# Optimization experiments

Measured on AMD Instinct MI355X. Metric: run time of the kernel, lower is better.

Reference implementation:

```python
import math
import jax
import jax.numpy as jnp
import numpy as np

N = 2_000_000
FOCAL = 1000.0
WIDTH = 1920.0
HEIGHT = 1080.0


def _quat_to_rot(q):
    # normalized quaternion (w, x, y, z) -> (N, 3, 3) rotation
    q = q / jnp.linalg.norm(q, axis=-1, keepdims=True)
    r, x, y, z = q[:, 0], q[:, 1], q[:, 2], q[:, 3]
    return jnp.stack([
        jnp.stack([1 - 2 * (y * y + z * z), 2 * (x * y - r * z), 2 * (x * z + r * y)], axis=-1),
        jnp.stack([2 * (x * y + r * z), 1 - 2 * (x * x + z * z), 2 * (y * z - r * x)], axis=-1),
        jnp.stack([2 * (x * z - r * y), 2 * (y * z + r * x), 1 - 2 * (x * x + y * y)], axis=-1),
    ], axis=1)


def _forward(points, quaternions, scales, colors, opacity, extrinsic, intrinsic,
             focal_x, focal_y, width, height, tile_size):
    fw, fh = float(width), float(height)
    # compute_fov_from_focal: fov = 2*atan(dim/(2*focal)); tan(fov/2)
    tan_fovX = math.tan(2.0 * math.atan(fw / (2.0 * focal_x)) / 2.0)
    tan_fovY = math.tan(2.0 * math.atan(fh / (2.0 * focal_y)) / 2.0)

    # 3D covariance: Sigma = (R S)(R S)^T
    R = _quat_to_rot(quaternions)
    M = R * scales[:, None, :]
    cov3d = M @ jnp.swapaxes(M, 1, 2)  # (N,3,3)

    ph = jnp.concatenate([points, jnp.ones_like(points[:, :1])], axis=1)  # (N,4)
    pc = ph @ extrinsic                         # camera space (N,4)
    zc = pc[:, 2]
    zmask = zc > 0.2
    z_safe = jnp.where(zmask, zc, 1.0)          # guard divisions for culled points
    x = jnp.clip(pc[:, 0] / z_safe, -1.3 * tan_fovX, 1.3 * tan_fovX) * zc
    y = jnp.clip(pc[:, 1] / z_safe, -1.3 * tan_fovY, 1.3 * tan_fovY) * zc

    zero = jnp.zeros_like(z_safe)
    j00 = focal_x / z_safe
    j02 = -(focal_x * x) / z_safe ** 2
    j11 = focal_y / z_safe
    j12 = -(focal_y * y) / z_safe ** 2
    J = jnp.stack([
        jnp.stack([j00, zero, j02], axis=-1),
        jnp.stack([zero, j11, j12], axis=-1),
        jnp.stack([zero, zero, zero], axis=-1)], axis=1)  # (N,3,3)

    Wm = extrinsic[:3, :3]
    T = jnp.einsum('ij,nkj->nik', Wm, J)        # W @ J^T, (N,3,3)
    C = jnp.swapaxes(T, 1, 2) @ jnp.swapaxes(cov3d, 1, 2) @ T
    a = C[:, 0, 0] + 0.3
    d = C[:, 1, 1] + 0.3
    b = C[:, 0, 1]
    c = C[:, 1, 0]
    cov2d = jnp.stack([jnp.stack([a, b], -1), jnp.stack([c, d], -1)], axis=1)  # (N,2,2)

    ndc = pc @ intrinsic
    w_safe = jnp.where(zmask, ndc[:, 3], 1.0)
    nx = ndc[:, 0] / w_safe
    ny = ndc[:, 1] / w_safe
    nz = ndc[:, 2]
    mask = (nz > 0.2) & (nx < 1.3) & (nx > -1.3) & (ny < 1.3) & (ny > -1.3)

    # analytic 2x2 inverse
    det = a * d - b * c
    det_safe = jnp.where(jnp.abs(det) < 1e-12, 1e-12, det)
    inv = jnp.stack([jnp.stack([d, -b], -1), jnp.stack([-c, a], -1)], axis=1) / det_safe[:, None, None]

    # radius from max eigenvalue of 2x2 covariance
    mid = 0.5 * (a + d)
    s = jnp.sqrt(jnp.maximum(mid * mid - det, 0.1))
    lmax = jnp.maximum(mid + s, mid - s)
    radius = jnp.ceil(3.0 * jnp.sqrt(jnp.maximum(lmax, 1e-6)))

    # ndc2Pix
    px = ((nx + 1.0) * fw - 1.0) * 0.5
    py = ((ny + 1.0) * fh - 1.0) * 0.5

    max_tx = math.ceil(fw / tile_size) - 1
    max_ty = math.ceil(fh / tile_size) - 1
    tlx = jnp.clip(((px - radius) / tile_size).astype(jnp.int32), 0, max_tx)
    tly = jnp.clip(((py - radius) / tile_size).astype(jnp.int32), 0, max_ty)
    brx = jnp.clip(((px + radius) / tile_size).astype(jnp.int32), 0, max_tx)
    bry = jnp.clip(((py + radius) / tile_size).astype(jnp.int32), 0, max_ty)
    span = jnp.maximum(brx + 1 - tlx, 1) * jnp.maximum(bry + 1 - tly, 1)
    tiles_touched = jnp.where(mask, span, 0)

    mean = jnp.stack([px, py, nz], axis=1)
    float_out = jnp.concatenate([
        mean,                      # 3: pixel-space mean + depth
        cov2d.reshape(-1, 4),      # 4
        inv.reshape(-1, 4),        # 4
        radius[:, None],           # 1
        colors,                    # 3
        opacity[:, None],          # 1
    ], axis=1)                     # (N,16)
    float_out = jnp.where(mask[:, None], float_out, 0.0)
    top_left = jnp.stack([tlx, tly])
    bottom_right = jnp.stack([brx, bry])
    return float_out, tiles_touched, top_left, bottom_right, mask


def setup_inputs() -> dict:
    key = jax.random.key(0)
    k = jax.random.split(key, 5)
    points = jax.random.normal(k[0], (N, 3), jnp.float32) * 2.0
    quaternions = jax.random.normal(k[1], (N, 4), jnp.float32)
    scales = jax.random.uniform(k[2], (N, 3), jnp.float32, 0.01, 0.1)
    colors = jax.random.uniform(k[3], (N, 3), jnp.float32)
    opacity = jax.random.normal(k[4], (N,), jnp.float32)
    # extrinsic is TRANSPOSED (translation in last row): camera 5 units back
    E = np.eye(4, dtype=np.float32)
    E[3, :3] = np.array([0.0, 0.0, 5.0], dtype=np.float32)
    # intrinsic (transposed OpenGL-style): w = z, z passed through
    tanX = WIDTH / (2.0 * FOCAL)
    tanY = HEIGHT / (2.0 * FOCAL)
    I = np.zeros((4, 4), dtype=np.float32)
    I[0, 0] = 1.0 / tanX
    I[1, 1] = 1.0 / tanY
    I[2, 2] = 1.0
    I[2, 3] = 1.0
    return {
        'points': points, 'quaternions': quaternions, 'scales': scales,
        'colors': colors, 'opacity': opacity,
        'extrinsic': jnp.asarray(E), 'intrinsic': jnp.asarray(I),
        'focal_x': 1000, 'focal_y': 1000, 'width': 1920, 'height': 1080,
        'tile_size': 16,
    }


def reference(points, quaternions, scales, colors, opacity, extrinsic, intrinsic,
              focal_x, focal_y, width, height, tile_size):
    return _forward(points, quaternions, scales, colors, opacity, extrinsic,
                    intrinsic, float(focal_x), float(focal_y), float(width),
                    float(height), int(tile_size))
```

## Files before the change

### kernel.cpp

```cpp
#include <hip/hip_runtime.h>
#include <math.h>

__global__ __launch_bounds__(256) void gs_fwd(
    const float* __restrict__ points,
    const float* __restrict__ quats,
    const float* __restrict__ scales,
    const float* __restrict__ colors,
    const float* __restrict__ opac,
    const float* __restrict__ E,
    const float* __restrict__ I,
    const int* __restrict__ p_fx,
    const int* __restrict__ p_fy,
    const int* __restrict__ p_w,
    const int* __restrict__ p_h,
    const int* __restrict__ p_tile,
    float* __restrict__ out,
    int N)
{
    const int i = blockIdx.x * blockDim.x + threadIdx.x;
    if (i >= N) return;

    const float fx = (float)p_fx[0];
    const float fy = (float)p_fy[0];
    const float fw = (float)p_w[0];
    const float fh = (float)p_h[0];
    const float ftile = (float)p_tile[0];
    const float rtile = __builtin_amdgcn_rcpf(ftile);

    const float tanX = fw / (2.0f * fx);
    const float tanY = fh / (2.0f * fy);
    const int max_tx = (int)ceilf(fw * rtile) - 1;
    const int max_ty = (int)ceilf(fh * rtile) - 1;

    const float4 q = reinterpret_cast<const float4*>(quats)[i];
    const float rq = rsqrtf(q.x*q.x + q.y*q.y + q.z*q.z + q.w*q.w);
    const float qr = q.x * rq;
    const float qx = q.y * rq;
    const float qy = q.z * rq;
    const float qz = q.w * rq;

    const float r00 = 1.0f - 2.0f * (qy*qy + qz*qz);
    const float r01 = 2.0f * (qx*qy - qr*qz);
    const float r02 = 2.0f * (qx*qz + qr*qy);
    const float r10 = 2.0f * (qx*qy + qr*qz);
    const float r11 = 1.0f - 2.0f * (qx*qx + qz*qz);
    const float r12 = 2.0f * (qy*qz - qr*qx);
    const float r20 = 2.0f * (qx*qz - qr*qy);
    const float r21 = 2.0f * (qy*qz + qr*qx);
    const float r22 = 1.0f - 2.0f * (qx*qx + qy*qy);

    const float s0 = scales[3*i + 0];
    const float s1 = scales[3*i + 1];
    const float s2 = scales[3*i + 2];

    const float m00 = r00*s0, m01 = r01*s1, m02 = r02*s2;
    const float m10 = r10*s0, m11 = r11*s1, m12 = r12*s2;
    const float m20 = r20*s0, m21 = r21*s1, m22 = r22*s2;

    const float S00 = m00*m00 + m01*m01 + m02*m02;
    const float S01 = m00*m10 + m01*m11 + m02*m12;
    const float S02 = m00*m20 + m01*m21 + m02*m22;
    const float S11 = m10*m10 + m11*m11 + m12*m12;
    const float S12 = m10*m20 + m11*m21 + m12*m22;
    const float S22 = m20*m20 + m21*m21 + m22*m22;

    const float p0 = points[3*i + 0];
    const float p1 = points[3*i + 1];
    const float p2 = points[3*i + 2];
    const float pc0 = p0*E[0]  + p1*E[4]  + p2*E[8]  + E[12];
    const float pc1 = p0*E[1]  + p1*E[5]  + p2*E[9]  + E[13];
    const float pc2 = p0*E[2]  + p1*E[6]  + p2*E[10] + E[14];
    const float pc3 = p0*E[3]  + p1*E[7]  + p2*E[11] + E[15];

    const float zc = pc2;
    const bool  zmask = zc > 0.2f;
    const float z_safe = zmask ? zc : 1.0f;
    const float rz = __builtin_amdgcn_rcpf(z_safe);

    const float limX = 1.3f * tanX;
    const float limY = 1.3f * tanY;
    const float xx = fminf(fmaxf(pc0 * rz, -limX), limX) * zc;
    const float yy = fminf(fmaxf(pc1 * rz, -limY), limY) * zc;

    const float j00 = fx * rz;
    const float j02 = -(fx * xx) * rz * rz;
    const float j11 = fy * rz;
    const float j12 = -(fy * yy) * rz * rz;

    const float t00 = E[0]*j00 + E[2]*j02;
    const float t01 = E[4]*j00 + E[6]*j02;
    const float t02 = E[8]*j00 + E[10]*j02;
    const float t10 = E[1]*j11 + E[2]*j12;
    const float t11 = E[5]*j11 + E[6]*j12;
    const float t12 = E[9]*j11 + E[10]*j12;

    const float v00 = S00*t00 + S01*t01 + S02*t02;
    const float v01 = S01*t00 + S11*t01 + S12*t02;
    const float v02 = S02*t00 + S12*t01 + S22*t02;
    const float v10 = S00*t10 + S01*t11 + S02*t12;
    const float v11 = S01*t10 + S11*t11 + S12*t12;
    const float v12 = S02*t10 + S12*t11 + S22*t12;

    const float a = (t00*v00 + t01*v01 + t02*v02) + 0.3f;
    const float b = (t00*v10 + t01*v11 + t02*v12);
    const float c = (t10*v00 + t11*v01 + t12*v02);
    const float d = (t10*v10 + t11*v11 + t12*v12) + 0.3f;

    const float n0 = pc0*I[0] + pc1*I[4] + pc2*I[8]  + pc3*I[12];
    const float n1 = pc0*I[1] + pc1*I[5] + pc2*I[9]  + pc3*I[13];
    const float n2 = pc0*I[2] + pc1*I[6] + pc2*I[10] + pc3*I[14];
    const float n3 = pc0*I[3] + pc1*I[7] + pc2*I[11] + pc3*I[15];

    const float w_safe = zmask ? n3 : 1.0f;
    const float rw = __builtin_amdgcn_rcpf(w_safe);
    const float nx = n0 * rw;
    const float ny = n1 * rw;
    const float nz = n2;

    const bool mask = (nz > 0.2f) && (nx < 1.3f) && (nx > -1.3f)
                                  && (ny < 1.3f) && (ny > -1.3f);
    const float fm = mask ? 1.0f : 0.0f;

    const float det = a*d - b*c;
    const float det_safe = (fabsf(det) < 1e-12f) ? 1e-12f : det;
    const float rdet = __builtin_amdgcn_rcpf(det_safe);
    const float inv00 =  d * rdet;
    const float inv01 = -b * rdet;
    const float inv10 = -c * rdet;
    const float inv11 =  a * rdet;

    const float mid = 0.5f * (a + d);
    const float sq  = sqrtf(fmaxf(mid*mid - det, 0.1f));
    const float lmax = fmaxf(mid + sq, mid - sq);
    const float radius = ceilf(3.0f * sqrtf(fmaxf(lmax, 1e-6f)));

    const float px = ((nx + 1.0f) * fw - 1.0f) * 0.5f;
    const float py = ((ny + 1.0f) * fh - 1.0f) * 0.5f;

    int tlx = (int)((px - radius) * rtile);
    int tly = (int)((py - radius) * rtile);
    int brx = (int)((px + radius) * rtile);
    int bry = (int)((py + radius) * rtile);
    tlx = min(max(tlx, 0), max_tx);
    tly = min(max(tly, 0), max_ty);
    brx = min(max(brx, 0), max_tx);
    bry = min(max(bry, 0), max_ty);

    const int sx = max(brx + 1 - tlx, 1);
    const int sy = max(bry + 1 - tly, 1);
    const float tiles = mask ? (float)(sx * sy) : 0.0f;

    const float c0 = colors[3*i + 0];
    const float c1 = colors[3*i + 1];
    const float c2 = colors[3*i + 2];
    const float op = opac[i];

    float4* row = reinterpret_cast<float4*>(out + (size_t)i * 16);
    row[0] = make_float4(px*fm, py*fm, nz*fm, a*fm);
    row[1] = make_float4(b*fm, c*fm, d*fm, inv00*fm);
    row[2] = make_float4(inv01*fm, inv10*fm, inv11*fm, radius*fm);
    row[3] = make_float4(c0*fm, c1*fm, c2*fm, op*fm);

    const size_t nb = (size_t)N;
    const size_t base = nb * 16;
    out[base + i]        = tiles;
    out[base + nb + i]   = (float)tlx;
    out[base + 2*nb + i] = (float)tly;
    out[base + 3*nb + i] = (float)brx;
    out[base + 4*nb + i] = (float)bry;
    out[base + 5*nb + i] = fm;
}

extern "C" void kernel_launch(void* const* d_in, const int* in_sizes, int n_in,
                              void* d_out, int out_size, void* d_ws, size_t ws_size,
                              hipStream_t stream) {
    const float* points = (const float*)d_in[0];
    const float* quats  = (const float*)d_in[1];
    const float* scales = (const float*)d_in[2];
    const float* colors = (const float*)d_in[3];
    const float* opac   = (const float*)d_in[4];
    const float* E      = (const float*)d_in[5];
    const float* I      = (const float*)d_in[6];
    const int* p_fx   = (const int*)d_in[7];
    const int* p_fy   = (const int*)d_in[8];
    const int* p_w    = (const int*)d_in[9];
    const int* p_h    = (const int*)d_in[10];
    const int* p_tile = (const int*)d_in[11];

    const int N = in_sizes[4];
    const int block = 256;
    const int grid = (N + block - 1) / block;
    gs_fwd<<<grid, block, 0, stream>>>(points, quats, scales, colors, opac,
                                       E, I, p_fx, p_fy, p_w, p_h, p_tile,
                                       (float*)d_out, N);
}
```

Baseline: 291.0 us.

## Process four gaussians per thread with float4 vectorized loads and stores

Each thread now handles four consecutive gaussians. Their 3-component inputs (points, scales, colors) and opacities are read as aligned float4 vectors, and the six planar outputs are written as float4 stores. This replaces the strided scalar 12-byte loads and scalar column stores with wide, coalesced memory transactions in a bandwidth-bound kernel. The cost is higher register pressure and a quarter as many threads, and a scalar fallback path remains for tails or N not divisible by four.

Result: slower. 366.7 us (+26.0%).

```diff
diff --git a/kernel.cpp b/kernel.cpp
--- a/kernel.cpp
+++ b/kernel.cpp
@@ -1,7 +1,135 @@
 #include <hip/hip_runtime.h>
 #include <math.h>
 
-__global__ __launch_bounds__(256) void gs_fwd(
+struct Plan { float tiles, tlx, tly, brx, bry, fm; };
+
+__device__ __forceinline__ Plan process_one(
+    float p0, float p1, float p2, float4 q,
+    float s0, float s1, float s2,
+    float c0, float c1, float c2, float op,
+    const float* __restrict__ E, const float* __restrict__ I,
+    float fx, float fy, float fw, float fh, float rtile,
+    float limX, float limY, int max_tx, int max_ty,
+    float4* __restrict__ rowptr)
+{
+    const float rq = rsqrtf(q.x*q.x + q.y*q.y + q.z*q.z + q.w*q.w);
+    const float qr = q.x * rq, qx = q.y * rq, qy = q.z * rq, qz = q.w * rq;
+
+    const float r00 = 1.0f - 2.0f * (qy*qy + qz*qz);
+    const float r01 = 2.0f * (qx*qy - qr*qz);
+    const float r02 = 2.0f * (qx*qz + qr*qy);
+    const float r10 = 2.0f * (qx*qy + qr*qz);
+    const float r11 = 1.0f - 2.0f * (qx*qx + qz*qz);
+    const float r12 = 2.0f * (qy*qz - qr*qx);
+    const float r20 = 2.0f * (qx*qz - qr*qy);
+    const float r21 = 2.0f * (qy*qz + qr*qx);
+    const float r22 = 1.0f - 2.0f * (qx*qx + qy*qy);
+
+    const float m00 = r00*s0, m01 = r01*s1, m02 = r02*s2;
+    const float m10 = r10*s0, m11 = r11*s1, m12 = r12*s2;
+    const float m20 = r20*s0, m21 = r21*s1, m22 = r22*s2;
+
+    const float S00 = m00*m00 + m01*m01 + m02*m02;
+    const float S01 = m00*m10 + m01*m11 + m02*m12;
+    const float S02 = m00*m20 + m01*m21 + m02*m22;
+    const float S11 = m10*m10 + m11*m11 + m12*m12;
+    const float S12 = m10*m20 + m11*m21 + m12*m22;
+    const float S22 = m20*m20 + m21*m21 + m22*m22;
+
+    const float pc0 = p0*E[0] + p1*E[4] + p2*E[8]  + E[12];
+    const float pc1 = p0*E[1] + p1*E[5] + p2*E[9]  + E[13];
+    const float pc2 = p0*E[2] + p1*E[6] + p2*E[10] + E[14];
+    const float pc3 = p0*E[3] + p1*E[7] + p2*E[11] + E[15];
+
+    const float zc = pc2;
+    const bool  zmask = zc > 0.2f;
+    const float z_safe = zmask ? zc : 1.0f;
+    const float rz = __builtin_amdgcn_rcpf(z_safe);
+
+    const float xx = fminf(fmaxf(pc0 * rz, -limX), limX) * zc;
+    const float yy = fminf(fmaxf(pc1 * rz, -limY), limY) * zc;
+
+    const float j00 = fx * rz;
+    const float j02 = -(fx * xx) * rz * rz;
+    const float j11 = fy * rz;
+    const float j12 = -(fy * yy) * rz * rz;
+
+    const float t00 = E[0]*j00 + E[2]*j02;
+    const float t01 = E[4]*j00 + E[6]*j02;
+    const float t02 = E[8]*j00 + E[10]*j02;
+    const float t10 = E[1]*j11 + E[2]*j12;
+    const float t11 = E[5]*j11 + E[6]*j12;
+    const float t12 = E[9]*j11 + E[10]*j12;
+
+    const float v00 = S00*t00 + S01*t01 + S02*t02;
+    const float v01 = S01*t00 + S11*t01 + S12*t02;
+    const float v02 = S02*t00 + S12*t01 + S22*t02;
+    const float v10 = S00*t10 + S01*t11 + S02*t12;
+    const float v11 = S01*t10 + S11*t11 + S12*t12;
+    const float v12 = S02*t10 + S12*t11 + S22*t12;
+
+    const float a = (t00*v00 + t01*v01 + t02*v02) + 0.3f;
+    const float b = (t00*v10 + t01*v11 + t02*v12);
+    const float c = (t10*v00 + t11*v01 + t12*v02);
+    const float d = (t10*v10 + t11*v11 + t12*v12) + 0.3f;
+
+    const float n0 = pc0*I[0] + pc1*I[4] + pc2*I[8]  + pc3*I[12];
+    const float n1 = pc0*I[1] + pc1*I[5] + pc2*I[9]  + pc3*I[13];
+    const float n2 = pc0*I[2] + pc1*I[6] + pc2*I[10] + pc3*I[14];
+    const float n3 = pc0*I[3] + pc1*I[7] + pc2*I[11] + pc3*I[15];
+
+    const float w_safe = zmask ? n3 : 1.0f;
+    const float rw = __builtin_amdgcn_rcpf(w_safe);
+    const float nx = n0 * rw;
+    const float ny = n1 * rw;
+    const float nz = n2;
+
+    const bool mask = (nz > 0.2f) && (nx < 1.3f) && (nx > -1.3f)
+                                  && (ny < 1.3f) && (ny > -1.3f);
+    const float fm = mask ? 1.0f : 0.0f;
+
+    const float det = a*d - b*c;
+    const float det_safe = (fabsf(det) < 1e-12f) ? 1e-12f : det;
+    const float rdet = __builtin_amdgcn_rcpf(det_safe);
+    const float inv00 =  d * rdet;
+    const float inv01 = -b * rdet;
+    const float inv10 = -c * rdet;
+    const float inv11 =  a * rdet;
+
+    const float mid = 0.5f * (a + d);
+    const float sq  = sqrtf(fmaxf(mid*mid - det, 0.1f));
+    const float lmax = fmaxf(mid + sq, mid - sq);
+    const float radius = ceilf(3.0f * sqrtf(fmaxf(lmax, 1e-6f)));
+
+    const float px = ((nx + 1.0f) * fw - 1.0f) * 0.5f;
+    const float py = ((ny + 1.0f) * fh - 1.0f) * 0.5f;
+
+    int tlx = (int)((px - radius) * rtile);
+    int tly = (int)((py - radius) * rtile);
+    int brx = (int)((px + radius) * rtile);
+    int bry = (int)((py + radius) * rtile);
+    tlx = min(max(tlx, 0), max_tx);
+    tly = min(max(tly, 0), max_ty);
+    brx = min(max(brx, 0), max_tx);
+    bry = min(max(bry, 0), max_ty);
+
+    const int sx = max(brx + 1 - tlx, 1);
+    const int sy = max(bry + 1 - tly, 1);
+
+    rowptr[0] = make_float4(px*fm, py*fm, nz*fm, a*fm);
+    rowptr[1] = make_float4(b*fm, c*fm, d*fm, inv00*fm);
+    rowptr[2] = make_float4(inv01*fm, inv10*fm, inv11*fm, radius*fm);
+    rowptr[3] = make_float4(c0*fm, c1*fm, c2*fm, op*fm);
+
+    Plan pl;
+    pl.tiles = mask ? (float)(sx * sy) : 0.0f;
+    pl.tlx = (float)tlx; pl.tly = (float)tly;
+    pl.brx = (float)brx; pl.bry = (float)bry;
+    pl.fm = fm;
+    return pl;
+}
+
+__global__ __launch_bounds__(256) void gs_fwd4(
     const float* __restrict__ points,
     const float* __restrict__ quats,
     const float* __restrict__ scales,
@@ -17,8 +145,9 @@
     float* __restrict__ out,
     int N)
 {
-    const int i = blockIdx.x * blockDim.x + threadIdx.x;
-    if (i >= N) return;
+    const int j = blockIdx.x * blockDim.x + threadIdx.x;
+    const int g0 = j * 4;
+    if (g0 >= N) return;
 
     const float fx = (float)p_fx[0];
     const float fy = (float)p_fy[0];
@@ -26,149 +155,73 @@
     const float fh = (float)p_h[0];
     const float ftile = (float)p_tile[0];
     const float rtile = __builtin_amdgcn_rcpf(ftile);
-
     const float tanX = fw / (2.0f * fx);
     const float tanY = fh / (2.0f * fy);
+    const float limX = 1.3f * tanX;
+    const float limY = 1.3f * tanY;
     const int max_tx = (int)ceilf(fw * rtile) - 1;
     const int max_ty = (int)ceilf(fh * rtile) - 1;
 
-    const float4 q = reinterpret_cast<const float4*>(quats)[i];
-    const float rq = rsqrtf(q.x*q.x + q.y*q.y + q.z*q.z + q.w*q.w);
-    const float qr = q.x * rq;
-    const float qx = q.y * rq;
-    const float qy = q.z * rq;
-    const float qz = q.w * rq;
-
-    const float r00 = 1.0f - 2.0f * (qy*qy + qz*qz);
-    const float r01 = 2.0f * (qx*qy - qr*qz);
-    const float r02 = 2.0f * (qx*qz + qr*qy);
-    const float r10 = 2.0f * (qx*qy + qr*qz);
-    const float r11 = 1.0f - 2.0f * (qx*qx + qz*qz);
-    const float r12 = 2.0f * (qy*qz - qr*qx);
-    const float r20 = 2.0f * (qx*qz - qr*qy);
-    const float r21 = 2.0f * (qy*qz + qr*qx);
-    const float r22 = 1.0f - 2.0f * (qx*qx + qy*qy);
-
-    const float s0 = scales[3*i + 0];
-    const float s1 = scales[3*i + 1];
-    const float s2 = scales[3*i + 2];
-
-    const float m00 = r00*s0, m01 = r01*s1, m02 = r02*s2;
-    const float m10 = r10*s0, m11 = r11*s1, m12 = r12*s2;
-    const float m20 = r20*s0, m21 = r21*s1, m22 = r22*s2;
-
-    const float S00 = m00*m00 + m01*m01 + m02*m02;
-    const float S01 = m00*m10 + m01*m11 + m02*m12;
-    const float S02 = m00*m20 + m01*m21 + m02*m22;
-    const float S11 = m10*m10 + m11*m11 + m12*m12;
-    const float S12 = m10*m20 + m11*m21 + m12*m22;
-    const float S22 = m20*m20 + m21*m21 + m22*m22;
-
-    const float p0 = points[3*i + 0];
-    const float p1 = points[3*i + 1];
-    const float p2 = points[3*i + 2];
-    const float pc0 = p0*E[0]  + p1*E[4]  + p2*E[8]  + E[12];
-    const float pc1 = p0*E[1]  + p1*E[5]  + p2*E[9]  + E[13];
-    const float pc2 = p0*E[2]  + p1*E[6]  + p2*E[10] + E[14];
-    const float pc3 = p0*E[3]  + p1*E[7]  + p2*E[11] + E[15];
-
-    const float zc = pc2;
-    const bool  zmask = zc > 0.2f;
-    const float z_safe = zmask ? zc : 1.0f;
-    const float rz = __builtin_amdgcn_rcpf(z_safe);
-
-    const float limX = 1.3f * tanX;
-    const float limY = 1.3f * tanY;
-    const float xx = fminf(fmaxf(pc0 * rz, -limX), limX) * zc;
-    const float yy = fminf(fmaxf(pc1 * rz, -limY), limY) * zc;
-
-    const float j00 = fx * rz;
-    const float j02 = -(fx * xx) * rz * rz;
-    const float j11 = fy * rz;
-    const float j12 = -(fy * yy) * rz * rz;
-
-    const float t00 = E[0]*j00 + E[2]*j02;
-    const float t01 = E[4]*j00 + E[6]*j02;
-    const float t02 = E[8]*j00 + E[10]*j02;
-    const float t10 = E[1]*j11 + E[2]*j12;
-    const float t11 = E[5]*j11 + E[6]*j12;
-    const float t12 = E[9]*j11 + E[10]*j12;
-
-    const float v00 = S00*t00 + S01*t01 + S02*t02;
-    const float v01 = S01*t00 + S11*t01 + S12*t02;
-    const float v02 = S02*t00 + S12*t01 + S22*t02;
-    const float v10 = S00*t10 + S01*t11 + S02*t12;
-    const float v11 = S01*t10 + S11*t11 + S12*t12;
-    const float v12 = S02*t10 + S12*t11 + S22*t12;
-
-    const float a = (t00*v00 + t01*v01 + t02*v02) + 0.3f;
-    const float b = (t00*v10 + t01*v11 + t02*v12);
-    const float c = (t10*v00 + t11*v01 + t12*v02);
-    const float d = (t10*v10 + t11*v11 + t12*v12) + 0.3f;
-
-    const float n0 = pc0*I[0] + pc1*I[4] + pc2*I[8]  + pc3*I[12];
-    const float n1 = pc0*I[1] + pc1*I[5] + pc2*I[9]  + pc3*I[13];
-    const float n2 = pc0*I[2] + pc1*I[6] + pc2*I[10] + pc3*I[14];
-    const float n3 = pc0*I[3] + pc1*I[7] + pc2*I[11] + pc3*I[15];
-
-    const float w_safe = zmask ? n3 : 1.0f;
-    const float rw = __builtin_amdgcn_rcpf(w_safe);
-    const float nx = n0 * rw;
-    const float ny = n1 * rw;
-    const float nz = n2;
-
-    const bool mask = (nz > 0.2f) && (nx < 1.3f) && (nx > -1.3f)
-                                  && (ny < 1.3f) && (ny > -1.3f);
-    const float fm = mask ? 1.0f : 0.0f;
-
-    const float det = a*d - b*c;
-    const float det_safe = (fabsf(det) < 1e-12f) ? 1e-12f : det;
-    const float rdet = __builtin_amdgcn_rcpf(det_safe);
-    const float inv00 =  d * rdet;
-    const float inv01 = -b * rdet;
-    const float inv10 = -c * rdet;
-    const float inv11 =  a * rdet;
-
-    const float mid = 0.5f * (a + d);
-    const float sq  = sqrtf(fmaxf(mid*mid - det, 0.1f));
-    const float lmax = fmaxf(mid + sq, mid - sq);
-    const float radius = ceilf(3.0f * sqrtf(fmaxf(lmax, 1e-6f)));
-
-    const float px = ((nx + 1.0f) * fw - 1.0f) * 0.5f;
-    const float py = ((ny + 1.0f) * fh - 1.0f) * 0.5f;
-
-    int tlx = (int)((px - radius) * rtile);
-    int tly = (int)((py - radius) * rtile);
-    int brx = (int)((px + radius) * rtile);
-    int bry = (int)((py + radius) * rtile);
-    tlx = min(max(tlx, 0), max_tx);
-    tly = min(max(tly, 0), max_ty);
-    brx = min(max(brx, 0), max_tx);
-    bry = min(max(bry, 0), max_ty);
-
-    const int sx = max(brx + 1 - tlx, 1);
-    const int sy = max(bry + 1 - tly, 1);
-    const float tiles = mask ? (float)(sx * sy) : 0.0f;
-
-    const float c0 = colors[3*i + 0];
-    const float c1 = colors[3*i + 1];
-    const float c2 = colors[3*i + 2];
-    const float op = opac[i];
-
-    float4* row = reinterpret_cast<float4*>(out + (size_t)i * 16);
-    row[0] = make_float4(px*fm, py*fm, nz*fm, a*fm);
-    row[1] = make_float4(b*fm, c*fm, d*fm, inv00*fm);
-    row[2] = make_float4(inv01*fm, inv10*fm, inv11*fm, radius*fm);
-    row[3] = make_float4(c0*fm, c1*fm, c2*fm, op*fm);
-
     const size_t nb = (size_t)N;
     const size_t base = nb * 16;
-    out[base + i]        = tiles;
-    out[base + nb + i]   = (float)tlx;
-    out[base + 2*nb + i] = (float)tly;
-    out[base + 3*nb + i] = (float)brx;
-    out[base + 4*nb + i] = (float)bry;
-    out[base + 5*nb + i] = fm;
+
+    if (g0 + 3 < N && (N & 3) == 0) {
+        const float4* P4 = reinterpret_cast<const float4*>(points);
+        const float4* Q4 = reinterpret_cast<const float4*>(quats);
+        const float4* S4 = reinterpret_cast<const float4*>(scales);
+        const float4* C4 = reinterpret_cast<const float4*>(colors);
+        const float4* O4 = reinterpret_cast<const float4*>(opac);
+
+        const float4 pA = P4[3*j], pB = P4[3*j+1], pC = P4[3*j+2];
+        const float4 q0v = Q4[4*j], q1v = Q4[4*j+1], q2v = Q4[4*j+2], q3v = Q4[4*j+3];
+        const float4 sA = S4[3*j], sB = S4[3*j+1], sC = S4[3*j+2];
+        const float4 cA = C4[3*j], cB = C4[3*j+1], cC = C4[3*j+2];
+        const float4 ov = O4[j];
+
+        float4* row = reinterpret_cast<float4*>(out + (size_t)g0 * 16);
+
+        Plan pl0 = process_one(pA.x, pA.y, pA.z, q0v, sA.x, sA.y, sA.z,
+                               cA.x, cA.y, cA.z, ov.x, E, I,
+                               fx, fy, fw, fh, rtile, limX, limY, max_tx, max_ty,
+                               row + 0);
+        Plan pl1 = process_one(pA.w, pB.x, pB.y, q1v, sA.w, sB.x, sB.y,
+                               cA.w, cB.x, cB.y, ov.y, E, I,
+                               fx, fy, fw, fh, rtile, limX, limY, max_tx, max_ty,
+                               row + 4);
+        Plan pl2 = process_one(pB.z, pB.w, pC.x, q2v, sB.z, sB.w, sC.x,
+                               cB.z, cB.w, cC.x, ov.z, E, I,
+                               fx, fy, fw, fh, rtile, limX, limY, max_tx, max_ty,
+                               row + 8);
+        Plan pl3 = process_one(pC.y, pC.z, pC.w, q3v, sC.y, sC.z, sC.w,
+                               cC.y, cC.z, cC.w, ov.w, E, I,
+                               fx, fy, fw, fh, rtile, limX, limY, max_tx, max_ty,
+                               row + 12);
+
+        float* ob = out + base;
+        reinterpret_cast<float4*>(ob)[j]          = make_float4(pl0.tiles, pl1.tiles, pl2.tiles, pl3.tiles);
+        reinterpret_cast<float4*>(ob + nb)[j]     = make_float4(pl0.tlx, pl1.tlx, pl2.tlx, pl3.tlx);
+        reinterpret_cast<float4*>(ob + 2*nb)[j]   = make_float4(pl0.tly, pl1.tly, pl2.tly, pl3.tly);
+        reinterpret_cast<float4*>(ob + 3*nb)[j]   = make_float4(pl0.brx, pl1.brx, pl2.brx, pl3.brx);
+        reinterpret_cast<float4*>(ob + 4*nb)[j]   = make_float4(pl0.bry, pl1.bry, pl2.bry, pl3.bry);
+        reinterpret_cast<float4*>(ob + 5*nb)[j]   = make_float4(pl0.fm, pl1.fm, pl2.fm, pl3.fm);
+    } else {
+        for (int i = g0; i < N && i < g0 + 4; ++i) {
+            const float4 q = make_float4(quats[4*i], quats[4*i+1], quats[4*i+2], quats[4*i+3]);
+            float4* row = reinterpret_cast<float4*>(out + (size_t)i * 16);
+            Plan pl = process_one(points[3*i], points[3*i+1], points[3*i+2], q,
+                                  scales[3*i], scales[3*i+1], scales[3*i+2],
+                                  colors[3*i], colors[3*i+1], colors[3*i+2],
+                                  opac[i], E, I,
+                                  fx, fy, fw, fh, rtile, limX, limY, max_tx, max_ty,
+                                  row);
+            out[base + i]        = pl.tiles;
+            out[base + nb + i]   = pl.tlx;
+            out[base + 2*nb + i] = pl.tly;
+            out[base + 3*nb + i] = pl.brx;
+            out[base + 4*nb + i] = pl.bry;
+            out[base + 5*nb + i] = pl.fm;
+        }
+    }
 }
 
 extern "C" void kernel_launch(void* const* d_in, const int* in_sizes, int n_in,
@@ -189,8 +242,9 @@
 
     const int N = in_sizes[4];
     const int block = 256;
-    const int grid = (N + block - 1) / block;
-    gs_fwd<<<grid, block, 0, stream>>>(points, quats, scales, colors, opac,
-                                       E, I, p_fx, p_fy, p_w, p_h, p_tile,
-                                       (float*)d_out, N);
+    const int nthreads = (N + 3) / 4;
+    const int grid = (nthreads + block - 1) / block;
+    gs_fwd4<<<grid, block, 0, stream>>>(points, quats, scales, colors, opac,
+                                        E, I, p_fx, p_fy, p_w, p_h, p_tile,
+                                        (float*)d_out, N);
 }
```
